# Kernel tuning notes

Measured on AMD Instinct MI355X. Metric: run time of the kernel, lower is better.

## Reference

```python
import jax, jax.numpy as jnp
import numpy as np

N_ATOM = 10000
D = 256
N_EDGE = 160000
BN_EPS = 1e-6


def _bn_eval(x, g, b, m, v):
    # BatchNorm1d in eval mode
    return (x - m) * jax.lax.rsqrt(v + BN_EPS) * g + b


def setup_inputs() -> dict:
    key = jax.random.key(0)
    ks = jax.random.split(key, 12)
    def glorot(k, shape):
        fan_in = shape[-1]
        return jax.random.normal(k, shape, dtype=jnp.float32) / np.sqrt(fan_in)
    inp = {
        'atom': jax.random.normal(ks[0], (N_ATOM, D), dtype=jnp.float32),
        'bond_index': jax.random.randint(ks[1], (2, N_EDGE), 0, N_ATOM, dtype=jnp.int32),
        # align: Linear(2D -> 1) + BN(1)
        'W_align': glorot(ks[2], (1, 2 * D)),
        'b_align': jnp.zeros((1,), jnp.float32),
        'bn_a_g': jnp.ones((1,), jnp.float32),
        'bn_a_b': jnp.zeros((1,), jnp.float32),
        'bn_a_m': jnp.zeros((1,), jnp.float32),
        'bn_a_v': jnp.ones((1,), jnp.float32),
        # attend: Linear(D -> D) + BN(D)
        'W_att': glorot(ks[3], (D, D)),
        'b_att': jnp.zeros((D,), jnp.float32),
        'bn_t_g': jnp.ones((D,), jnp.float32),
        'bn_t_b': jnp.zeros((D,), jnp.float32),
        'bn_t_m': jnp.zeros((D,), jnp.float32),
        'bn_t_v': jnp.ones((D,), jnp.float32),
        # GRUCell(D, D): weights stacked [r; z; n] as in torch
        'W_ih': glorot(ks[4], (3 * D, D)),
        'W_hh': glorot(ks[5], (3 * D, D)),
        'b_ih': jnp.zeros((3 * D,), jnp.float32),
        'b_hh': jnp.zeros((3 * D,), jnp.float32),
    }
    return inp


def reference(atom, bond_index, W_align, b_align, bn_a_g, bn_a_b, bn_a_m, bn_a_v,
              W_att, b_att, bn_t_g, bn_t_b, bn_t_m, bn_t_v,
              W_ih, W_hh, b_ih, b_hh):
    num_atom = atom.shape[0]
    src = bond_index[0]
    dst = bond_index[1]

    # gather + concat: [E, 2D]
    feat_align = jnp.concatenate([atom[src], atom[dst]], axis=-1)
    # align score: Linear(2D->1) + BN + leaky_relu -> [E, 1]
    s = feat_align @ W_align.T + b_align
    s = _bn_eval(s, bn_a_g, bn_a_b, bn_a_m, bn_a_v)
    s = jax.nn.leaky_relu(s, negative_slope=0.01)

    # segment softmax over edges grouped by src atom
    seg_max = jax.ops.segment_max(s, src, num_segments=num_atom)  # [N, 1]
    e = jnp.exp(s - seg_max[src])
    denom = jax.ops.segment_sum(e, src, num_segments=num_atom)    # [N, 1]
    attn = e / (denom[src] + 1e-8)                                # [E, 1]

    # attend: Linear(D->D) + BN on gathered dst features
    h = atom[dst] @ W_att.T + b_att
    h = _bn_eval(h, bn_t_g, bn_t_b, bn_t_m, bn_t_v)

    # weighted scatter-add aggregation -> [N, D], then ELU
    context = jax.ops.segment_sum(attn * h, src, num_segments=num_atom)
    context = jax.nn.elu(context)

    # GRUCell: input=context, hidden=atom
    gi = context @ W_ih.T + b_ih   # [N, 3D]
    gh = atom @ W_hh.T + b_hh      # [N, 3D]
    i_r, i_z, i_n = jnp.split(gi, 3, axis=-1)
    h_r, h_z, h_n = jnp.split(gh, 3, axis=-1)
    r = jax.nn.sigmoid(i_r + h_r)
    z = jax.nn.sigmoid(i_z + h_z)
    n = jnp.tanh(i_n + r * h_n)
    update = (1.0 - z) * n + z * atom
    return update
```

## Files before the change

kernel.cpp:

```cpp
#include <hip/hip_runtime.h>
#include <hip/hip_bf16.h>

#define D 256

typedef __attribute__((ext_vector_type(8))) short bf16x8;
typedef __attribute__((ext_vector_type(4))) short s16x4;
typedef __attribute__((ext_vector_type(4))) float f32x4;

#define MFMA __builtin_amdgcn_mfma_f32_16x16x32_bf16

__device__ __forceinline__ float s2f(short u) {
    union { unsigned int i; float f; } c;
    c.i = ((unsigned int)(unsigned short)u) << 16;
    return c.f;
}
__device__ __forceinline__ short f2s(float f) {
    union { float f; unsigned int u; } c; c.f = f;
    unsigned int u = c.u;
    u += 0x7fffu + ((u >> 16) & 1u);
    return (short)(u >> 16);
}

__global__ __launch_bounds__(256) void prep_kernel(
    const float* __restrict__ atom, short* __restrict__ atom_bf,
    const float* __restrict__ W_align, const float* __restrict__ b_align,
    const float* __restrict__ g, const float* __restrict__ bb,
    const float* __restrict__ mn, const float* __restrict__ vr,
    float* __restrict__ p0p, float* __restrict__ p1p,
    const float* __restrict__ Wa, short* __restrict__ Wa_bf,
    const float* __restrict__ Wi, short* __restrict__ Wi_bf,
    const float* __restrict__ Wh, short* __restrict__ Wh_bf,
    int* __restrict__ cnt, int* __restrict__ cursor,
    int N, int NROWB, int WCVTB)
{
    int b = blockIdx.x, tid = threadIdx.x;
    if (b < NROWB) {
        int wave = tid >> 6, lane = tid & 63;
        int row = b * 4 + wave;
        if (row >= N) return;
        float4 a = *(const float4*)(atom + (size_t)row * D + lane * 4);
        s16x4 o; o[0] = f2s(a.x); o[1] = f2s(a.y); o[2] = f2s(a.z); o[3] = f2s(a.w);
        ((s16x4*)(atom_bf + (size_t)row * D))[lane] = o;
        float4 w0 = *(const float4*)(W_align + lane * 4);
        float4 w1 = *(const float4*)(W_align + D + lane * 4);
        float d0 = a.x * w0.x + a.y * w0.y + a.z * w0.z + a.w * w0.w;
        float d1 = a.x * w1.x + a.y * w1.y + a.z * w1.z + a.w * w1.w;
        #pragma unroll
        for (int s = 32; s > 0; s >>= 1) {
            d0 += __shfl_xor(d0, s, 64);
            d1 += __shfl_xor(d1, s, 64);
        }
        if (lane == 0) {
            float A = rsqrtf(vr[0] + 1e-6f) * g[0];
            p0p[row] = A * (d0 + b_align[0]) + bb[0] - A * mn[0];
            p1p[row] = A * d1;
        }
        return;
    }
    b -= NROWB;
    if (b < WCVTB) {
        int nW4 = D * D / 4, nG4 = 3 * D * D / 4;
        int j = b * 256 + tid;
        const float* src; short* dst;
        if (j < nW4) { src = Wa; dst = Wa_bf; }
        else { j -= nW4;
            if (j < nG4) { src = Wi; dst = Wi_bf; }
            else { j -= nG4;
                if (j < nG4) { src = Wh; dst = Wh_bf; }
                else return;
            }
        }
        float4 v = ((const float4*)src)[j];
        s16x4 o; o[0] = f2s(v.x); o[1] = f2s(v.y); o[2] = f2s(v.z); o[3] = f2s(v.w);
        ((s16x4*)dst)[j] = o;
        return;
    }
    b -= WCVTB;
    int i = b * 256 + tid;
    if (i < N) { cnt[i] = 0; cursor[i] = 0; }
}

__global__ __launch_bounds__(256) void count_kernel(const int* __restrict__ src, int* cnt, int E) {
    int e = blockIdx.x * 256 + threadIdx.x;
    if (e < E) atomicAdd(&cnt[src[e]], 1);
}

__global__ __launch_bounds__(1024) void scan_kernel(const int* __restrict__ cnt, int* __restrict__ off, int N) {
    __shared__ int sums[1024];
    int t = threadIdx.x;
    int CH = (N + 1023) / 1024;
    int beg = t * CH;
    int end = beg + CH; if (end > N) end = N;
    int s = 0;
    for (int i = beg; i < end; i++) s += cnt[i];
    sums[t] = s;
    __syncthreads();
    for (int d = 1; d < 1024; d <<= 1) {
        int x = (t >= d) ? sums[t - d] : 0;
        __syncthreads();
        sums[t] += x;
        __syncthreads();
    }
    int run = (t > 0) ? sums[t - 1] : 0;
    for (int i = beg; i < end; i++) { off[i] = run; run += cnt[i]; }
    if (end == N) off[N] = run;
}

__global__ __launch_bounds__(256) void fill_kernel(const int* __restrict__ src, const int* __restrict__ dst,
                                                   const int* __restrict__ off, int* cursor, int* dlist, int E) {
    int e = blockIdx.x * 256 + threadIdx.x;
    if (e < E) {
        int s = src[e];
        int p = atomicAdd(&cursor[s], 1);
        dlist[off[s] + p] = dst[e];
    }
}

__global__ __launch_bounds__(256) void hA_kernel(
    const short* __restrict__ atom_bf, const short* __restrict__ W_bf,
    const float* __restrict__ bias,
    const float* __restrict__ g, const float* __restrict__ bb,
    const float* __restrict__ mn, const float* __restrict__ vr,
    short* __restrict__ hA, int N, int NB)
{
    __shared__ short Bs[2048 * 8];
    int bi = blockIdx.x;
    int xcd = bi & 7, rest = bi >> 3;
    int cb = rest & 3, gh = rest >> 2;
    int gg = gh * 8 + xcd;
    if (gg >= NB) return;
    int c0 = cb * 64;
    int tid = threadIdx.x;
    for (int c = tid; c < 2048; c += 256) {
        int l15c = c & 15, quadc = (c >> 4) & 3, t2 = c >> 6;
        int kkc = t2 & 7, jc = t2 >> 3;
        bf16x8 v = *(const bf16x8*)(W_bf + (size_t)(c0 + jc * 16 + l15c) * D + quadc * 8 + kkc * 32);
        *(bf16x8*)(&Bs[c * 8]) = v;
    }
    __syncthreads();

    int wave = tid >> 6, lane = tid & 63;
    int quad = lane >> 4, l15 = lane & 15;
    int m0 = gg * 128 + wave * 16;
    int ar0 = m0 + l15;       if (ar0 > N - 1) ar0 = N - 1;
    int ar1 = m0 + 64 + l15;  if (ar1 > N - 1) ar1 = N - 1;
    const short* ap0 = atom_bf + (size_t)ar0 * D + quad * 8;
    const short* ap1 = atom_bf + (size_t)ar1 * D + quad * 8;
    const short* lb = &Bs[lane * 8];
    f32x4 acc[2][4];
    #pragma unroll
    for (int t = 0; t < 2; t++)
        #pragma unroll
        for (int j = 0; j < 4; j++) acc[t][j] = (f32x4){0,0,0,0};
    #pragma unroll
    for (int kk = 0; kk < 8; kk++) {
        int k = kk * 32;
        bf16x8 a0 = *(const bf16x8*)(ap0 + k);
        bf16x8 a1 = *(const bf16x8*)(ap1 + k);
        bf16x8 b0 = *(const bf16x8*)(lb + (0 * 8 + kk) * 512);
        bf16x8 b1 = *(const bf16x8*)(lb + (1 * 8 + kk) * 512);
        bf16x8 b2 = *(const bf16x8*)(lb + (2 * 8 + kk) * 512);
        bf16x8 b3 = *(const bf16x8*)(lb + (3 * 8 + kk) * 512);
        acc[0][0] = MFMA(a0, b0, acc[0][0], 0, 0, 0);
        acc[0][1] = MFMA(a0, b1, acc[0][1], 0, 0, 0);
        acc[0][2] = MFMA(a0, b2, acc[0][2], 0, 0, 0);
        acc[0][3] = MFMA(a0, b3, acc[0][3], 0, 0, 0);
        acc[1][0] = MFMA(a1, b0, acc[1][0], 0, 0, 0);
        acc[1][1] = MFMA(a1, b1, acc[1][1], 0, 0, 0);
        acc[1][2] = MFMA(a1, b2, acc[1][2], 0, 0, 0);
        acc[1][3] = MFMA(a1, b3, acc[1][3], 0, 0, 0);
    }
    #pragma unroll
    for (int j = 0; j < 4; j++) {
        int col = c0 + j * 16 + l15;
        float sc = rsqrtf(vr[col] + 1e-6f) * g[col];
        float sh = bb[col] - mn[col] * sc;
        float bi_ = bias[col];
        #pragma unroll
        for (int t = 0; t < 2; t++) {
            #pragma unroll
            for (int r = 0; r < 4; r++) {
                int row = m0 + t * 64 + quad * 4 + r;
                if (row < N) hA[(size_t)row * D + col] = f2s((acc[t][j][r] + bi_) * sc + sh);
            }
        }
    }
}

__global__ __launch_bounds__(256) void agg_kernel(
    const int* __restrict__ off, const int* __restrict__ dlist,
    const float* __restrict__ p0p, const float* __restrict__ p1p,
    const short* __restrict__ hA, short* __restrict__ ctx, int N)
{
    int w = (blockIdx.x * blockDim.x + threadIdx.x) >> 6;
    int lane = threadIdx.x & 63;
    if (w >= N) return;
    int beg = off[w], end = off[w + 1];
    float u = p0p[w];
    float m = -INFINITY;
    for (int j = beg + lane; j < end; j += 64) {
        float x = u + p1p[dlist[j]];
        x = x > 0.f ? x : 0.01f * x;
        m = fmaxf(m, x);
    }
    #pragma unroll
    for (int o = 32; o > 0; o >>= 1) m = fmaxf(m, __shfl_xor(m, o, 64));
    float sum = 0.f;
    for (int j = beg + lane; j < end; j += 64) {
        float x = u + p1p[dlist[j]];
        x = x > 0.f ? x : 0.01f * x;
        sum += __expf(x - m);
    }
    #pragma unroll
    for (int o = 32; o > 0; o >>= 1) sum += __shfl_xor(sum, o, 64);
    float inv = 1.f / (sum + 1e-8f);
    int half = lane >> 5, l32 = lane & 31;
    float acc[8] = {0.f,0.f,0.f,0.f,0.f,0.f,0.f,0.f};
    for (int j = beg + half; j < end; j += 2) {
        int d = dlist[j];
        float x = u + p1p[d];
        x = x > 0.f ? x : 0.01f * x;
        float coef = __expf(x - m) * inv;
        bf16x8 h = *(const bf16x8*)(hA + (size_t)d * D + l32 * 8);
        #pragma unroll
        for (int i = 0; i < 8; i++) acc[i] += coef * s2f(h[i]);
    }
    #pragma unroll
    for (int i = 0; i < 8; i++) acc[i] += __shfl_xor(acc[i], 32, 64);
    if (half == 0) {
        bf16x8 o;
        #pragma unroll
        for (int i = 0; i < 8; i++) {
            float v = acc[i];
            v = v > 0.f ? v : __expf(v) - 1.f;
            o[i] = f2s(v);
        }
        *(bf16x8*)(ctx + (size_t)w * D + l32 * 8) = o;
    }
}

__global__ __launch_bounds__(256) void gru_kernel(
    const short* __restrict__ ctx, const short* __restrict__ atom_bf,
    const short* __restrict__ W_ih, const short* __restrict__ W_hh,
    const float* __restrict__ b_ih, const float* __restrict__ b_hh,
    float* __restrict__ out, int N, int NB)
{
    __shared__ short Bs[3072 * 8];
    int bi = blockIdx.x;
    int xcd = bi & 7, rest = bi >> 3;
    int cb = rest & 15, gh = rest >> 4;
    int gg = gh * 8 + xcd;
    if (gg >= NB) return;
    int c0 = cb * 16;
    int tid = threadIdx.x;
    for (int c = tid; c < 3072; c += 256) {
        int l15c = c & 15, quadc = (c >> 4) & 3, t2 = c >> 6;
        int kkc = t2 & 7, gate = t2 >> 3;
        const short* srcp = (gate < 3)
            ? W_ih + (size_t)(gate * 256 + c0 + l15c) * D + quadc * 8 + kkc * 32
            : W_hh + (size_t)((gate - 3) * 256 + c0 + l15c) * D + quadc * 8 + kkc * 32;
        *(bf16x8*)(&Bs[c * 8]) = *(const bf16x8*)srcp;
    }
    __syncthreads();

    int wave = tid >> 6, lane = tid & 63;
    int quad = lane >> 4, l15 = lane & 15;
    int m0 = gg * 128 + wave * 16;
    int ar0 = m0 + l15;       if (ar0 > N - 1) ar0 = N - 1;
    int ar1 = m0 + 64 + l15;  if (ar1 > N - 1) ar1 = N - 1;
    const short* cp0 = ctx + (size_t)ar0 * D + quad * 8;
    const short* ap0 = atom_bf + (size_t)ar0 * D + quad * 8;
    const short* cp1 = ctx + (size_t)ar1 * D + quad * 8;
    const short* ap1 = atom_bf + (size_t)ar1 * D + quad * 8;
    const short* lb = &Bs[lane * 8];
    f32x4 gi[2][3], gh_[2][3];
    #pragma unroll
    for (int t = 0; t < 2; t++)
        #pragma unroll
        for (int j = 0; j < 3; j++) { gi[t][j] = (f32x4){0,0,0,0}; gh_[t][j] = (f32x4){0,0,0,0}; }
    #pragma unroll
    for (int kk = 0; kk < 8; kk++) {
        int k = kk * 32;
        bf16x8 c0v = *(const bf16x8*)(cp0 + k);
        bf16x8 a0v = *(const bf16x8*)(ap0 + k);
        bf16x8 c1v = *(const bf16x8*)(cp1 + k);
        bf16x8 a1v = *(const bf16x8*)(ap1 + k);
        bf16x8 bir = *(const bf16x8*)(lb + (0 * 8 + kk) * 512);
        bf16x8 biz = *(const bf16x8*)(lb + (1 * 8 + kk) * 512);
        bf16x8 bin = *(const bf16x8*)(lb + (2 * 8 + kk) * 512);
        bf16x8 bhr = *(const bf16x8*)(lb + (3 * 8 + kk) * 512);
        bf16x8 bhz = *(const bf16x8*)(lb + (4 * 8 + kk) * 512);
        bf16x8 bhn = *(const bf16x8*)(lb + (5 * 8 + kk) * 512);
        gi[0][0] = MFMA(c0v, bir, gi[0][0], 0, 0, 0);
        gi[0][1] = MFMA(c0v, biz, gi[0][1], 0, 0, 0);
        gi[0][2] = MFMA(c0v, bin, gi[0][2], 0, 0, 0);
        gh_[0][0] = MFMA(a0v, bhr, gh_[0][0], 0, 0, 0);
        gh_[0][1] = MFMA(a0v, bhz, gh_[0][1], 0, 0, 0);
        gh_[0][2] = MFMA(a0v, bhn, gh_[0][2], 0, 0, 0);
        gi[1][0] = MFMA(c1v, bir, gi[1][0], 0, 0, 0);
        gi[1][1] = MFMA(c1v, biz, gi[1][1], 0, 0, 0);
        gi[1][2] = MFMA(c1v, bin, gi[1][2], 0, 0, 0);
        gh_[1][0] = MFMA(a1v, bhr, gh_[1][0], 0, 0, 0);
        gh_[1][1] = MFMA(a1v, bhz, gh_[1][1], 0, 0, 0);
        gh_[1][2] = MFMA(a1v, bhn, gh_[1][2], 0, 0, 0);
    }
    int col = c0 + l15;
    float bir_s = b_ih[col], biz_s = b_ih[col + 256], bin_s = b_ih[col + 512];
    float bhr_s = b_hh[col], bhz_s = b_hh[col + 256], bhn_s = b_hh[col + 512];
    #pragma unroll
    for (int t = 0; t < 2; t++) {
        #pragma unroll
        for (int r = 0; r < 4; r++) {
            int row = m0 + t * 64 + quad * 4 + r;
            if (row < N) {
                float rr = 1.f / (1.f + __expf(-(gi[t][0][r] + bir_s + gh_[t][0][r] + bhr_s)));
                float zz = 1.f / (1.f + __expf(-(gi[t][1][r] + biz_s + gh_[t][1][r] + bhz_s)));
                float nn = tanhf(gi[t][2][r] + bin_s + rr * (gh_[t][2][r] + bhn_s));
                float at = s2f(atom_bf[(size_t)row * D + col]);
                out[(size_t)row * D + col] = (1.f - zz) * nn + zz * at;
            }
        }
    }
}

extern "C" void kernel_launch(void* const* d_in, const int* in_sizes, int n_in,
                              void* d_out, int out_size, void* d_ws, size_t ws_size,
                              hipStream_t stream) {
    const float* atom    = (const float*)d_in[0];
    const int*   bond    = (const int*)d_in[1];
    const float* W_align = (const float*)d_in[2];
    const float* b_align = (const float*)d_in[3];
    const float* bn_a_g  = (const float*)d_in[4];
    const float* bn_a_b  = (const float*)d_in[5];
    const float* bn_a_m  = (const float*)d_in[6];
    const float* bn_a_v  = (const float*)d_in[7];
    const float* W_att   = (const float*)d_in[8];
    const float* b_att   = (const float*)d_in[9];
    const float* bn_t_g  = (const float*)d_in[10];
    const float* bn_t_b  = (const float*)d_in[11];
    const float* bn_t_m  = (const float*)d_in[12];
    const float* bn_t_v  = (const float*)d_in[13];
    const float* W_ih    = (const float*)d_in[14];
    const float* W_hh    = (const float*)d_in[15];
    const float* b_ih    = (const float*)d_in[16];
    const float* b_hh    = (const float*)d_in[17];

    int N = in_sizes[0] / D;
    int E = in_sizes[1] / 2;
    const int* src = bond;
    const int* dst = bond + E;

    char* w = (char*)d_ws;
    size_t o = 0;
    auto alloc = [&](size_t bytes) {
        void* p = w + o;
        o = (o + bytes + 255) & ~(size_t)255;
        return p;
    };
    int*   cnt     = (int*)alloc((size_t)N * 4);
    int*   cursor  = (int*)alloc((size_t)N * 4);
    int*   offv    = (int*)alloc((size_t)(N + 1) * 4);
    int*   dlist   = (int*)alloc((size_t)E * 4);
    float* p0p     = (float*)alloc((size_t)N * 4);
    float* p1p     = (float*)alloc((size_t)N * 4);
    short* hA      = (short*)alloc((size_t)N * D * 2);
    short* ctx     = (short*)alloc((size_t)N * D * 2);
    short* atom_bf = (short*)alloc((size_t)N * D * 2);
    short* Watt_bf = (short*)alloc((size_t)D * D * 2);
    short* Wih_bf  = (short*)alloc((size_t)3 * D * D * 2);
    short* Whh_bf  = (short*)alloc((size_t)3 * D * D * 2);

    int NROWB = (N + 3) / 4;
    int nWtot4 = (D * D + 2 * 3 * D * D) / 4;
    int WCVTB = (nWtot4 + 255) / 256;
    int INITB = (N + 255) / 256;
    prep_kernel<<<NROWB + WCVTB + INITB, 256, 0, stream>>>(
        atom, atom_bf, W_align, b_align, bn_a_g, bn_a_b, bn_a_m, bn_a_v, p0p, p1p,
        W_att, Watt_bf, W_ih, Wih_bf, W_hh, Whh_bf, cnt, cursor, N, NROWB, WCVTB);
    count_kernel<<<(E + 255) / 256, 256, 0, stream>>>(src, cnt, E);
    scan_kernel<<<1, 1024, 0, stream>>>(cnt, offv, N);
    fill_kernel<<<(E + 255) / 256, 256, 0, stream>>>(src, dst, offv, cursor, dlist, E);

    int NB = (N + 127) / 128;
    int GH = (NB + 7) / 8;
    hA_kernel<<<8 * 4 * GH, 256, 0, stream>>>(
        atom_bf, Watt_bf, b_att, bn_t_g, bn_t_b, bn_t_m, bn_t_v, hA, N, NB);
    agg_kernel<<<((size_t)N * 64 + 255) / 256, 256, 0, stream>>>(
        offv, dlist, p0p, p1p, hA, ctx, N);
    gru_kernel<<<8 * 16 * GH, 256, 0, stream>>>(
        ctx, atom_bf, Wih_bf, Whh_bf, b_ih, b_hh, (float*)d_out, N, NB);
}
```

Baseline: 195.4 us.

## Merge prep, count, scan and fill into one cooperative kernel with grid syncs

Replaces four separate launches (prep, count, scan, fill) with a single cooperative kernel of 256 blocks that loops over the virtual prep blocks and separates the phases with grid.sync(). This is meant to cut launch overhead and the inter-kernel gaps in the short CSR-building front end. In exchange, the prep work and the edge loops run on only 256 blocks, and the scan now uses 256 threads instead of 1024, so each thread sums about 40 counts serially. Each grid barrier also has its own cost.

```diff
diff --git a/kernel.cpp b/kernel.cpp
--- a/kernel.cpp
+++ b/kernel.cpp
@@ -1,5 +1,8 @@
 #include <hip/hip_runtime.h>
 #include <hip/hip_bf16.h>
+#include <hip/hip_cooperative_groups.h>
+
+namespace cg = cooperative_groups;
 
 #define D 256
 
@@ -21,7 +24,7 @@
     return (short)(u >> 16);
 }
 
-__global__ __launch_bounds__(256) void prep_kernel(
+__global__ __launch_bounds__(256) void front_kernel(
     const float* __restrict__ atom, short* __restrict__ atom_bf,
     const float* __restrict__ W_align, const float* __restrict__ b_align,
     const float* __restrict__ g, const float* __restrict__ bb,
@@ -31,88 +34,94 @@
     const float* __restrict__ Wi, short* __restrict__ Wi_bf,
     const float* __restrict__ Wh, short* __restrict__ Wh_bf,
     int* __restrict__ cnt, int* __restrict__ cursor,
-    int N, int NROWB, int WCVTB)
+    int* __restrict__ offv, int* __restrict__ dlist,
+    const int* __restrict__ src, const int* __restrict__ dst,
+    int N, int E, int NROWB, int WCVTB, int TOTB)
 {
-    int b = blockIdx.x, tid = threadIdx.x;
-    if (b < NROWB) {
-        int wave = tid >> 6, lane = tid & 63;
-        int row = b * 4 + wave;
-        if (row >= N) return;
-        float4 a = *(const float4*)(atom + (size_t)row * D + lane * 4);
-        s16x4 o; o[0] = f2s(a.x); o[1] = f2s(a.y); o[2] = f2s(a.z); o[3] = f2s(a.w);
-        ((s16x4*)(atom_bf + (size_t)row * D))[lane] = o;
-        float4 w0 = *(const float4*)(W_align + lane * 4);
-        float4 w1 = *(const float4*)(W_align + D + lane * 4);
-        float d0 = a.x * w0.x + a.y * w0.y + a.z * w0.z + a.w * w0.w;
-        float d1 = a.x * w1.x + a.y * w1.y + a.z * w1.z + a.w * w1.w;
-        #pragma unroll
-        for (int s = 32; s > 0; s >>= 1) {
-            d0 += __shfl_xor(d0, s, 64);
-            d1 += __shfl_xor(d1, s, 64);
-        }
-        if (lane == 0) {
-            float A = rsqrtf(vr[0] + 1e-6f) * g[0];
-            p0p[row] = A * (d0 + b_align[0]) + bb[0] - A * mn[0];
-            p1p[row] = A * d1;
-        }
-        return;
-    }
-    b -= NROWB;
-    if (b < WCVTB) {
-        int nW4 = D * D / 4, nG4 = 3 * D * D / 4;
-        int j = b * 256 + tid;
-        const float* src; short* dst;
-        if (j < nW4) { src = Wa; dst = Wa_bf; }
-        else { j -= nW4;
-            if (j < nG4) { src = Wi; dst = Wi_bf; }
-            else { j -= nG4;
-                if (j < nG4) { src = Wh; dst = Wh_bf; }
-                else return;
+    __shared__ int sums[256];
+    cg::grid_group grid = cg::this_grid();
+    int tid = threadIdx.x;
+
+    for (int vb = blockIdx.x; vb < TOTB; vb += gridDim.x) {
+        int b = vb;
+        if (b < NROWB) {
+            int wave = tid >> 6, lane = tid & 63;
+            int row = b * 4 + wave;
+            if (row < N) {
+                float4 a = *(const float4*)(atom + (size_t)row * D + lane * 4);
+                s16x4 o; o[0] = f2s(a.x); o[1] = f2s(a.y); o[2] = f2s(a.z); o[3] = f2s(a.w);
+                ((s16x4*)(atom_bf + (size_t)row * D))[lane] = o;
+                float4 w0 = *(const float4*)(W_align + lane * 4);
+                float4 w1 = *(const float4*)(W_align + D + lane * 4);
+                float d0 = a.x * w0.x + a.y * w0.y + a.z * w0.z + a.w * w0.w;
+                float d1 = a.x * w1.x + a.y * w1.y + a.z * w1.z + a.w * w1.w;
+                #pragma unroll
+                for (int s = 32; s > 0; s >>= 1) {
+                    d0 += __shfl_xor(d0, s, 64);
+                    d1 += __shfl_xor(d1, s, 64);
+                }
+                if (lane == 0) {
+                    float A = rsqrtf(vr[0] + 1e-6f) * g[0];
+                    p0p[row] = A * (d0 + b_align[0]) + bb[0] - A * mn[0];
+                    p1p[row] = A * d1;
+                }
+            }
+        } else {
+            b -= NROWB;
+            if (b < WCVTB) {
+                int nW4 = D * D / 4, nG4 = 3 * D * D / 4;
+                int j = b * 256 + tid;
+                const float* sp = 0; short* dp = 0;
+                if (j < nW4) { sp = Wa; dp = Wa_bf; }
+                else { j -= nW4;
+                    if (j < nG4) { sp = Wi; dp = Wi_bf; }
+                    else { j -= nG4;
+                        if (j < nG4) { sp = Wh; dp = Wh_bf; }
+                    }
+                }
+                if (sp) {
+                    float4 v = ((const float4*)sp)[j];
+                    s16x4 o; o[0] = f2s(v.x); o[1] = f2s(v.y); o[2] = f2s(v.z); o[3] = f2s(v.w);
+                    ((s16x4*)dp)[j] = o;
+                }
+            } else {
+                b -= WCVTB;
+                int i = b * 256 + tid;
+                if (i < N) { cnt[i] = 0; cursor[i] = 0; }
             }
         }
-        float4 v = ((const float4*)src)[j];
-        s16x4 o; o[0] = f2s(v.x); o[1] = f2s(v.y); o[2] = f2s(v.z); o[3] = f2s(v.w);
-        ((s16x4*)dst)[j] = o;
-        return;
-    }
-    b -= WCVTB;
-    int i = b * 256 + tid;
-    if (i < N) { cnt[i] = 0; cursor[i] = 0; }
-}
-
-__global__ __launch_bounds__(256) void count_kernel(const int* __restrict__ src, int* cnt, int E) {
-    int e = blockIdx.x * 256 + threadIdx.x;
-    if (e < E) atomicAdd(&cnt[src[e]], 1);
-}
-
-__global__ __launch_bounds__(1024) void scan_kernel(const int* __restrict__ cnt, int* __restrict__ off, int N) {
-    __shared__ int sums[1024];
-    int t = threadIdx.x;
-    int CH = (N + 1023) / 1024;
-    int beg = t * CH;
-    int end = beg + CH; if (end > N) end = N;
-    int s = 0;
-    for (int i = beg; i < end; i++) s += cnt[i];
-    sums[t] = s;
-    __syncthreads();
-    for (int d = 1; d < 1024; d <<= 1) {
-        int x = (t >= d) ? sums[t - d] : 0;
+    }
+    grid.sync();
+
+    for (int e = blockIdx.x * 256 + tid; e < E; e += gridDim.x * 256)
+        atomicAdd(&cnt[src[e]], 1);
+    grid.sync();
+
+    if (blockIdx.x == 0) {
+        int CH = (N + 255) / 256;
+        int beg = tid * CH;
+        int end = beg + CH; if (end > N) end = N;
+        if (beg > N) beg = N;
+        int s = 0;
+        for (int i = beg; i < end; i++) s += cnt[i];
+        sums[tid] = s;
         __syncthreads();
-        sums[t] += x;
-        __syncthreads();
-    }
-    int run = (t > 0) ? sums[t - 1] : 0;
-    for (int i = beg; i < end; i++) { off[i] = run; run += cnt[i]; }
-    if (end == N) off[N] = run;
-}
-
-__global__ __launch_bounds__(256) void fill_kernel(const int* __restrict__ src, const int* __restrict__ dst,
-                                                   const int* __restrict__ off, int* cursor, int* dlist, int E) {
-    int e = blockIdx.x * 256 + threadIdx.x;
-    if (e < E) {
+        for (int d = 1; d < 256; d <<= 1) {
+            int x = (tid >= d) ? sums[tid - d] : 0;
+            __syncthreads();
+            sums[tid] += x;
+            __syncthreads();
+        }
+        int run = (tid > 0) ? sums[tid - 1] : 0;
+        for (int i = beg; i < end; i++) { offv[i] = run; run += cnt[i]; }
+        if (end == N) offv[N] = run;
+    }
+    grid.sync();
+
+    for (int e = blockIdx.x * 256 + tid; e < E; e += gridDim.x * 256) {
         int s = src[e];
         int p = atomicAdd(&cursor[s], 1);
-        dlist[off[s] + p] = dst[e];
+        dlist[offv[s] + p] = dst[e];
     }
 }
 
@@ -374,12 +383,19 @@
     int nWtot4 = (D * D + 2 * 3 * D * D) / 4;
     int WCVTB = (nWtot4 + 255) / 256;
     int INITB = (N + 255) / 256;
-    prep_kernel<<<NROWB + WCVTB + INITB, 256, 0, stream>>>(
-        atom, atom_bf, W_align, b_align, bn_a_g, bn_a_b, bn_a_m, bn_a_v, p0p, p1p,
-        W_att, Watt_bf, W_ih, Wih_bf, W_hh, Whh_bf, cnt, cursor, N, NROWB, WCVTB);
-    count_kernel<<<(E + 255) / 256, 256, 0, stream>>>(src, cnt, E);
-    scan_kernel<<<1, 1024, 0, stream>>>(cnt, offv, N);
-    fill_kernel<<<(E + 255) / 256, 256, 0, stream>>>(src, dst, offv, cursor, dlist, E);
+    int TOTB = NROWB + WCVTB + INITB;
+
+    void* args[] = {
+        (void*)&atom, (void*)&atom_bf, (void*)&W_align, (void*)&b_align,
+        (void*)&bn_a_g, (void*)&bn_a_b, (void*)&bn_a_m, (void*)&bn_a_v,
+        (void*)&p0p, (void*)&p1p,
+        (void*)&W_att, (void*)&Watt_bf, (void*)&W_ih, (void*)&Wih_bf,
+        (void*)&W_hh, (void*)&Whh_bf,
+        (void*)&cnt, (void*)&cursor, (void*)&offv, (void*)&dlist,
+        (void*)&src, (void*)&dst,
+        (void*)&N, (void*)&E, (void*)&NROWB, (void*)&WCVTB, (void*)&TOTB
+    };
+    hipLaunchCooperativeKernel((void*)front_kernel, dim3(256), dim3(256), args, 0, stream);
 
     int NB = (N + 127) / 128;
     int GH = (NB + 7) / 8;
```

Result: slower. 319.5 us (+63.5%).
